# Kernel tuning notes

Hardware: AMD Instinct MI355X
Metric: run time of the kernel (lower is better)

Reference implementation:

```python
import jax, jax.numpy as jnp
import numpy as np

C = 64          # channels
L = 2           # GRU layers
DEC_STEPS = 35


def setup_inputs() -> dict:
    key = jax.random.key(0)
    ks = jax.random.split(key, 10)
    B, S = 2048, 512
    s = 0.1  # small init scale keeps gates in linear-ish region
    return {
        "pulse":    jax.random.normal(ks[0], (B, S, 2), dtype=jnp.float32),
        "dense1_w": jax.random.normal(ks[1], (C, 2), dtype=jnp.float32) * s,
        "dense1_b": jax.random.normal(ks[2], (C,), dtype=jnp.float32) * s,
        "dense2_w": jax.random.normal(ks[3], (2, C), dtype=jnp.float32) * s,
        "dense2_b": jax.random.normal(ks[4], (2,), dtype=jnp.float32) * s,
        "Wih":      jax.random.normal(ks[5], (L, 3 * C, C), dtype=jnp.float32) * s,
        "Whh":      jax.random.normal(ks[6], (L, 3 * C, C), dtype=jnp.float32) * s,
        "bih":      jax.random.normal(ks[7], (L, 3 * C), dtype=jnp.float32) * s,
        "bhh":      jax.random.normal(ks[8], (L, 3 * C), dtype=jnp.float32) * s,
        "embed":    jax.random.normal(ks[9], (1, C), dtype=jnp.float32) * s,
    }


def _gru_cell(x, h, wih, whh, bi, bh):
    # PyTorch GRU cell math (gate order r, z, n)
    gi = x @ wih.T + bi   # [B, 3C]
    gh = h @ whh.T + bh   # [B, 3C]
    ir, iz, inn = jnp.split(gi, 3, axis=-1)
    hr, hz, hn = jnp.split(gh, 3, axis=-1)
    r = jax.nn.sigmoid(ir + hr)
    z = jax.nn.sigmoid(iz + hz)
    n = jnp.tanh(inn + r * hn)
    return (1.0 - z) * n + z * h


def _multi_step(h_stack, x, Wih, Whh, bih, bhh):
    # One timestep through L stacked GRU layers. h_stack: [L, B, C]
    new_h = []
    inp = x
    for l in range(L):
        hl = _gru_cell(inp, h_stack[l], Wih[l], Whh[l], bih[l], bhh[l])
        new_h.append(hl)
        inp = hl
    return jnp.stack(new_h), inp  # (new state stack, top-layer output)


def reference(pulse, dense1_w, dense1_b, dense2_w, dense2_b, Wih, Whh, bih, bhh, embed):
    B = pulse.shape[0]
    # dense1 then time-major [S, B, C]
    x = pulse @ dense1_w.T + dense1_b
    x = jnp.transpose(x, (1, 0, 2))
    h0 = jnp.zeros((L, B, C), dtype=x.dtype)

    def enc_step(h, xt):
        h2, _ = _multi_step(h, xt, Wih, Whh, bih, bhh)
        return h2, None

    hT, _ = jax.lax.scan(enc_step, h0, x)  # encoder final state [L, B, C]

    sos = jnp.broadcast_to(embed[0], (B, C))  # embedding of token 0

    def dec_step(carry, _):
        latest, h = carry
        h2, out = _multi_step(h, latest, Wih, Whh, bih, bhh)
        return (out, h2), out

    _, outs = jax.lax.scan(dec_step, (sos, hT), None, length=DEC_STEPS)  # [35, B, C]

    # dense2 on decoder outputs; slicing pred[:, 1:, :] in the source drops the
    # sos position, which equals applying dense2 to the 35 decoder outputs only.
    pred = jnp.transpose(outs, (1, 0, 2)) @ dense2_w.T + dense2_b  # [B, 35, 2]
    return pred
```

## Files before the change

kernel.cpp:

```cpp
#include <hip/hip_runtime.h>
#include <math.h>


#define CCH  64
#define GG   192
#define SEQ  512
#define DECS 35
#define BT   8
#define NTH  512
#define NW   8
#define RSTR 20
#define STG_SH  (16 * 17 * 8)

typedef __attribute__((ext_vector_type(8))) short bf16x8;
typedef __attribute__((ext_vector_type(4))) float f32x4;

__device__ __forceinline__ short f2b(float f) {
  union { float f; unsigned u; } v; v.f = f;
  unsigned r = v.u + 0x7fffu + ((v.u >> 16) & 1u);
  return (short)(r >> 16);
}
__device__ __forceinline__ float sigf(float x) { return 1.0f / (1.0f + __expf(-x)); }
__device__ __forceinline__ float tanhfast(float x) {
  float t = __expf(-2.0f * fabsf(x));
  float r = (1.0f - t) / (1.0f + t);
  return copysignf(r, x);
}
__device__ __forceinline__ int stoff(int row, int k) {
  return ((k >> 3) * 17 + row) * 8 + (k & 7);
}

extern "C" __global__ void __launch_bounds__(NTH, 2)
gru_fused2(const float* __restrict__ pulse,
           const float* __restrict__ d1w,
           const float* __restrict__ d1b,
           const float* __restrict__ d2w,
           const float* __restrict__ d2b,
           const float* __restrict__ Wih,
           const float* __restrict__ Whh,
           const float* __restrict__ bih,
           const float* __restrict__ bhh,
           const float* __restrict__ embed,
           float* __restrict__ out)
{
  __shared__ __align__(16) unsigned short stA[STG_SH];
  __shared__ __align__(16) unsigned short stC[STG_SH];
  __shared__ __align__(16) float scr[NW * 32 * RSTR];
  __shared__ float red[NW * 16];

  const int tid = threadIdx.x;
  const int wid = tid >> 6;
  const int l   = tid & 63;
  const int lm  = l & 15;
  const int lg  = l >> 4;
  const int ob  = l >> 3;
  const int ocl = l & 7;
  const int och = wid * 8 + ocl;
  const int bgb = blockIdx.x * BT;

  for (int i = tid; i < STG_SH; i += NTH) { stA[i] = 0; stC[i] = 0; }

  const float* Wih0 = Wih;
  const float* Whh0 = Whh;
  const float* Wih1 = Wih + GG * CCH;
  const float* Whh1 = Whh + GG * CCH;
  bf16x8 bA[2][4], bC[2][4];
#pragma unroll
  for (int t = 0; t < 2; ++t) {
    const int cc = t * 16 + lm;
    const int g  = cc >> 3;
    const int ch = wid * 8 + (cc & 7);
#pragma unroll
    for (int s = 0; s < 4; ++s) {
#pragma unroll
      for (int e = 0; e < 8; ++e) {
        int kk = 32 * s + 8 * lg + e;
        float va = 0.f, vc = 0.f;
        if (g < 3) {
          int row = g * CCH + ch;
          va = (kk < 64) ? Wih0[row * CCH + kk] : Whh0[row * CCH + kk - 64];
          vc = (kk < 64) ? Wih1[row * CCH + kk] : Whh1[row * CCH + kk - 64];
        }
        bA[t][s][e] = f2b(va);
        bC[t][s][e] = f2b(vc);
      }
    }
  }

  float A0[3], A1[3], C0[3], bi0_[3], bh0_[3], bi1_[3], bh1_[3];
#pragma unroll
  for (int g = 0; g < 3; ++g) {
    int row = g * CCH + och;
    float a0 = 0.f, a1 = 0.f, cc = 0.f;
    for (int k = 0; k < CCH; ++k) {
      float wv = Wih0[row * CCH + k];
      a0 += wv * d1w[2 * k];
      a1 += wv * d1w[2 * k + 1];
      cc += wv * d1b[k];
    }
    A0[g] = a0; A1[g] = a1; C0[g] = cc + bih[row];
    bi0_[g] = bih[row];      bh0_[g] = bhh[row];
    bi1_[g] = bih[GG + row]; bh1_[g] = bhh[GG + row];
  }
  const float w20 = d2w[och], w21 = d2w[CCH + och];
  const float o_b0 = d2b[0], o_b1 = d2b[1];
  float h0 = 0.f, h1 = 0.f;
  short hb0 = 0, hb1 = 0;

  float* ws = scr + wid * 32 * RSTR;
  __syncthreads();

  for (int t = 0; t < SEQ; ++t) {
    stC[stoff(8 + ob, 64 + och)] = hb1;
    float2 pv = *(const float2*)(pulse + ((size_t)(bgb + ob) * SEQ + t) * 2);
    {
      f32x4 a0 = {0.f, 0.f, 0.f, 0.f}, a1 = {0.f, 0.f, 0.f, 0.f};
#pragma unroll
      for (int s = 2; s < 4; ++s) {
        bf16x8 af = *(const bf16x8*)&stA[((s * 4 + lg) * 17 + lm) * 8];
        a0 = __builtin_amdgcn_mfma_f32_16x16x32_bf16(af, bA[0][s], a0, 0, 0, 0);
        a1 = __builtin_amdgcn_mfma_f32_16x16x32_bf16(af, bA[1][s], a1, 0, 0, 0);
      }
      *(f32x4*)(ws + (0 * 16 + lm) * RSTR + lg * 4) = a0;
      *(f32x4*)(ws + (1 * 16 + lm) * RSTR + lg * 4) = a1;
    }
    {
      float ghR = ws[(0 * 8 + ocl) * RSTR + 8 + ob];
      float ghZ = ws[(1 * 8 + ocl) * RSTR + 8 + ob];
      float ghN = ws[(2 * 8 + ocl) * RSTR + 8 + ob];
      float giR = pv.x * A0[0] + pv.y * A1[0] + C0[0];
      float giZ = pv.x * A0[1] + pv.y * A1[1] + C0[1];
      float giN = pv.x * A0[2] + pv.y * A1[2] + C0[2];
      float r = sigf(giR + ghR + bh0_[0]);
      float z = sigf(giZ + ghZ + bh0_[1]);
      float nn = tanhfast(giN + r * (ghN + bh0_[2]));
      h0 = (1.f - z) * nn + z * h0;
      hb0 = f2b(h0);
      stC[stoff(ob, och)] = hb0;
    }
    __syncthreads();

    stA[stoff(8 + ob, 64 + och)] = hb0;
    {
      f32x4 a0 = {0.f, 0.f, 0.f, 0.f}, a1 = {0.f, 0.f, 0.f, 0.f};
#pragma unroll
      for (int s = 0; s < 4; ++s) {
        bf16x8 af = *(const bf16x8*)&stC[((s * 4 + lg) * 17 + lm) * 8];
        a0 = __builtin_amdgcn_mfma_f32_16x16x32_bf16(af, bC[0][s], a0, 0, 0, 0);
        a1 = __builtin_amdgcn_mfma_f32_16x16x32_bf16(af, bC[1][s], a1, 0, 0, 0);
      }
      *(f32x4*)(ws + (0 * 16 + lm) * RSTR + lg * 4) = a0;
      *(f32x4*)(ws + (1 * 16 + lm) * RSTR + lg * 4) = a1;
    }
    {
      float aR = ws[(0 * 8 + ocl) * RSTR + ob];
      float aZ = ws[(1 * 8 + ocl) * RSTR + ob];
      float aN = ws[(2 * 8 + ocl) * RSTR + ob];
      float hR = ws[(0 * 8 + ocl) * RSTR + 8 + ob];
      float hZ = ws[(1 * 8 + ocl) * RSTR + 8 + ob];
      float hN = ws[(2 * 8 + ocl) * RSTR + 8 + ob];
      float r = sigf(aR + hR + bi1_[0] + bh1_[0]);
      float z = sigf(aZ + hZ + bi1_[1] + bh1_[1]);
      float nn = tanhfast(aN + bi1_[2] + r * (hN + bh1_[2]));
      h1 = (1.f - z) * nn + z * h1;
      hb1 = f2b(h1);
    }
    __syncthreads();
  }

  stA[stoff(ob, och)] = f2b(embed[och]);
  __syncthreads();

  for (int d = 0; d < DECS; ++d) {
    stC[stoff(8 + ob, 64 + och)] = hb1;
    if (wid == 0 && l < 16 && d > 0) {
      int b = l >> 1, o = l & 1;
      float s = 0.f;
#pragma unroll
      for (int w = 0; w < NW; ++w) s += red[w * 16 + b * 2 + o];
      out[((size_t)(bgb + b) * DECS + (d - 1)) * 2 + o] = s + (o ? o_b1 : o_b0);
    }
    {
      f32x4 a0 = {0.f, 0.f, 0.f, 0.f}, a1 = {0.f, 0.f, 0.f, 0.f};
#pragma unroll
      for (int s = 0; s < 4; ++s) {
        bf16x8 af = *(const bf16x8*)&stA[((s * 4 + lg) * 17 + lm) * 8];
        a0 = __builtin_amdgcn_mfma_f32_16x16x32_bf16(af, bA[0][s], a0, 0, 0, 0);
        a1 = __builtin_amdgcn_mfma_f32_16x16x32_bf16(af, bA[1][s], a1, 0, 0, 0);
      }
      *(f32x4*)(ws + (0 * 16 + lm) * RSTR + lg * 4) = a0;
      *(f32x4*)(ws + (1 * 16 + lm) * RSTR + lg * 4) = a1;
    }
    {
      float aR = ws[(0 * 8 + ocl) * RSTR + ob];
      float aZ = ws[(1 * 8 + ocl) * RSTR + ob];
      float aN = ws[(2 * 8 + ocl) * RSTR + ob];
      float hR = ws[(0 * 8 + ocl) * RSTR + 8 + ob];
      float hZ = ws[(1 * 8 + ocl) * RSTR + 8 + ob];
      float hN = ws[(2 * 8 + ocl) * RSTR + 8 + ob];
      float r = sigf(aR + hR + bi0_[0] + bh0_[0]);
      float z = sigf(aZ + hZ + bi0_[1] + bh0_[1]);
      float nn = tanhfast(aN + bi0_[2] + r * (hN + bh0_[2]));
      h0 = (1.f - z) * nn + z * h0;
      hb0 = f2b(h0);
      stC[stoff(ob, och)] = hb0;
    }
    __syncthreads();

    stA[stoff(8 + ob, 64 + och)] = hb0;
    {
      f32x4 a0 = {0.f, 0.f, 0.f, 0.f}, a1 = {0.f, 0.f, 0.f, 0.f};
#pragma unroll
      for (int s = 0; s < 4; ++s) {
        bf16x8 af = *(const bf16x8*)&stC[((s * 4 + lg) * 17 + lm) * 8];
        a0 = __builtin_amdgcn_mfma_f32_16x16x32_bf16(af, bC[0][s], a0, 0, 0, 0);
        a1 = __builtin_amdgcn_mfma_f32_16x16x32_bf16(af, bC[1][s], a1, 0, 0, 0);
      }
      *(f32x4*)(ws + (0 * 16 + lm) * RSTR + lg * 4) = a0;
      *(f32x4*)(ws + (1 * 16 + lm) * RSTR + lg * 4) = a1;
    }
    {
      float aR = ws[(0 * 8 + ocl) * RSTR + ob];
      float aZ = ws[(1 * 8 + ocl) * RSTR + ob];
      float aN = ws[(2 * 8 + ocl) * RSTR + ob];
      float hR = ws[(0 * 8 + ocl) * RSTR + 8 + ob];
      float hZ = ws[(1 * 8 + ocl) * RSTR + 8 + ob];
      float hN = ws[(2 * 8 + ocl) * RSTR + 8 + ob];
      float r = sigf(aR + hR + bi1_[0] + bh1_[0]);
      float z = sigf(aZ + hZ + bi1_[1] + bh1_[1]);
      float nn = tanhfast(aN + bi1_[2] + r * (hN + bh1_[2]));
      h1 = (1.f - z) * nn + z * h1;
      hb1 = f2b(h1);
      stA[stoff(ob, och)] = hb1;
      float p0 = h1 * w20, p1 = h1 * w21;
      p0 += __shfl_xor(p0, 1); p0 += __shfl_xor(p0, 2); p0 += __shfl_xor(p0, 4);
      p1 += __shfl_xor(p1, 1); p1 += __shfl_xor(p1, 2); p1 += __shfl_xor(p1, 4);
      if (ocl == 0) {
        red[wid * 16 + ob * 2 + 0] = p0;
        red[wid * 16 + ob * 2 + 1] = p1;
      }
    }
    __syncthreads();
  }

  if (wid == 0 && l < 16) {
    int b = l >> 1, o = l & 1;
    float s = 0.f;
#pragma unroll
    for (int w = 0; w < NW; ++w) s += red[w * 16 + b * 2 + o];
    out[((size_t)(bgb + b) * DECS + (DECS - 1)) * 2 + o] = s + (o ? o_b1 : o_b0);
  }
}

extern "C" void kernel_launch(void* const* d_in, const int* in_sizes, int n_in,
                              void* d_out, int out_size, void* d_ws, size_t ws_size,
                              hipStream_t stream) {
  const float* pulse = (const float*)d_in[0];
  const float* d1w   = (const float*)d_in[1];
  const float* d1b   = (const float*)d_in[2];
  const float* d2w   = (const float*)d_in[3];
  const float* d2b   = (const float*)d_in[4];
  const float* Wih   = (const float*)d_in[5];
  const float* Whh   = (const float*)d_in[6];
  const float* bih   = (const float*)d_in[7];
  const float* bhh   = (const float*)d_in[8];
  const float* emb   = (const float*)d_in[9];
  float* out = (float*)d_out;

  int B = in_sizes[0] / (SEQ * 2);
  gru_fused2<<<B / BT, NTH, 0, stream>>>(pulse, d1w, d1b, d2w, d2b,
                                         Wih, Whh, bih, bhh, emb, out);
}
```

Baseline: 607.8 us.

## Swap MFMA operands so gate outputs land in lanes, dropping LDS scratch

The MFMA operands are swapped (weights as A, hidden state as B), and the weight rows are permuted so each lane's accumulator holds the r, z and n gate pre-activations for one channel and batch element. This removes the per-step round trip through the LDS scratch buffer (store the accumulators, then gather them back) in both GRU layers. In exchange the hidden state is written twice into the staging buffer, because the 8 batch rows are duplicated across 16 columns, which halves useful MFMA throughput. Biases are also pre-summed. Numerics change slightly because the layer-1 input and hidden r/z terms are now summed inside the MFMA.

```diff
diff --git a/kernel.cpp b/kernel.cpp
--- a/kernel.cpp
+++ b/kernel.cpp
@@ -9,8 +9,7 @@
 #define BT   8
 #define NTH  512
 #define NW   8
-#define RSTR 20
-#define STG_SH  (16 * 17 * 8)
+#define STG_SH (16 * 17 * 8)
 
 typedef __attribute__((ext_vector_type(8))) short bf16x8;
 typedef __attribute__((ext_vector_type(4))) float f32x4;
@@ -26,26 +25,25 @@
   float r = (1.0f - t) / (1.0f + t);
   return copysignf(r, x);
 }
-__device__ __forceinline__ int stoff(int row, int k) {
-  return ((k >> 3) * 17 + row) * 8 + (k & 7);
+__device__ __forceinline__ int stoff(int col, int k) {
+  return ((k >> 3) * 17 + col) * 8 + (k & 7);
 }
 
 extern "C" __global__ void __launch_bounds__(NTH, 2)
-gru_fused2(const float* __restrict__ pulse,
-           const float* __restrict__ d1w,
-           const float* __restrict__ d1b,
-           const float* __restrict__ d2w,
-           const float* __restrict__ d2b,
-           const float* __restrict__ Wih,
-           const float* __restrict__ Whh,
-           const float* __restrict__ bih,
-           const float* __restrict__ bhh,
-           const float* __restrict__ embed,
-           float* __restrict__ out)
+gru_lane(const float* __restrict__ pulse,
+         const float* __restrict__ d1w,
+         const float* __restrict__ d1b,
+         const float* __restrict__ d2w,
+         const float* __restrict__ d2b,
+         const float* __restrict__ Wih,
+         const float* __restrict__ Whh,
+         const float* __restrict__ bih,
+         const float* __restrict__ bhh,
+         const float* __restrict__ embed,
+         float* __restrict__ out)
 {
   __shared__ __align__(16) unsigned short stA[STG_SH];
   __shared__ __align__(16) unsigned short stC[STG_SH];
-  __shared__ __align__(16) float scr[NW * 32 * RSTR];
   __shared__ float red[NW * 16];
 
   const int tid = threadIdx.x;
@@ -53,9 +51,8 @@
   const int l   = tid & 63;
   const int lm  = l & 15;
   const int lg  = l >> 4;
-  const int ob  = l >> 3;
-  const int ocl = l & 7;
-  const int och = wid * 8 + ocl;
+  const int b   = lm & 7;
+  const int ch  = wid * 8 + ((lm >> 3) << 2) + lg;
   const int bgb = blockIdx.x * BT;
 
   for (int i = tid; i < STG_SH; i += NTH) { stA[i] = 0; stC[i] = 0; }
@@ -64,22 +61,27 @@
   const float* Whh0 = Whh;
   const float* Wih1 = Wih + GG * CCH;
   const float* Whh1 = Whh + GG * CCH;
+  const int sub = lm & 3;
   bf16x8 bA[2][4], bC[2][4];
 #pragma unroll
   for (int t = 0; t < 2; ++t) {
-    const int cc = t * 16 + lm;
-    const int g  = cc >> 3;
-    const int ch = wid * 8 + (cc & 7);
+    const int wch = wid * 8 + t * 4 + (lm >> 2);
+    const int rr  = (sub == 0 ? wch : (sub == 1 ? 64 + wch : 128 + wch));
 #pragma unroll
     for (int s = 0; s < 4; ++s) {
 #pragma unroll
       for (int e = 0; e < 8; ++e) {
         int kk = 32 * s + 8 * lg + e;
-        float va = 0.f, vc = 0.f;
-        if (g < 3) {
-          int row = g * CCH + ch;
-          va = (kk < 64) ? Wih0[row * CCH + kk] : Whh0[row * CCH + kk - 64];
-          vc = (kk < 64) ? Wih1[row * CCH + kk] : Whh1[row * CCH + kk - 64];
+        float va, vc;
+        if (sub == 2) {
+          va = kk < 64 ? Wih0[rr * CCH + kk] : 0.f;
+          vc = kk < 64 ? Wih1[rr * CCH + kk] : 0.f;
+        } else if (sub == 3) {
+          va = kk < 64 ? 0.f : Whh0[rr * CCH + kk - 64];
+          vc = kk < 64 ? 0.f : Whh1[rr * CCH + kk - 64];
+        } else {
+          va = kk < 64 ? Wih0[rr * CCH + kk] : Whh0[rr * CCH + kk - 64];
+          vc = kk < 64 ? Wih1[rr * CCH + kk] : Whh1[rr * CCH + kk - 64];
         }
         bA[t][s][e] = f2b(va);
         bC[t][s][e] = f2b(vc);
@@ -87,10 +89,10 @@
     }
   }
 
-  float A0[3], A1[3], C0[3], bi0_[3], bh0_[3], bi1_[3], bh1_[3];
+  float A0f[3], A1f[3], C0f[3];
 #pragma unroll
   for (int g = 0; g < 3; ++g) {
-    int row = g * CCH + och;
+    int row = g * CCH + ch;
     float a0 = 0.f, a1 = 0.f, cc = 0.f;
     for (int k = 0; k < CCH; ++k) {
       float wv = Wih0[row * CCH + k];
@@ -98,157 +100,140 @@
       a1 += wv * d1w[2 * k + 1];
       cc += wv * d1b[k];
     }
-    A0[g] = a0; A1[g] = a1; C0[g] = cc + bih[row];
-    bi0_[g] = bih[row];      bh0_[g] = bhh[row];
-    bi1_[g] = bih[GG + row]; bh1_[g] = bhh[GG + row];
-  }
-  const float w20 = d2w[och], w21 = d2w[CCH + och];
-  const float o_b0 = d2b[0], o_b1 = d2b[1];
+    A0f[g] = a0; A1f[g] = a1; C0f[g] = cc + bih[row];
+  }
+  const float bh0r = bhh[ch], bh0z = bhh[64 + ch], bh0n = bhh[128 + ch];
+  const float b0r = bih[ch] + bh0r, b0z = bih[64 + ch] + bh0z;
+  const float bi0n = bih[128 + ch];
+  const float b1r = bih[GG + ch] + bhh[GG + ch];
+  const float b1z = bih[GG + 64 + ch] + bhh[GG + 64 + ch];
+  const float bi1n = bih[GG + 128 + ch], bh1n = bhh[GG + 128 + ch];
+  const float w2a = d2w[ch], w2b = d2w[CCH + ch];
+  const float d2b0 = d2b[0], d2b1 = d2b[1];
   float h0 = 0.f, h1 = 0.f;
   short hb0 = 0, hb1 = 0;
 
-  float* ws = scr + wid * 32 * RSTR;
+  const float* prow = pulse + (size_t)(bgb + b) * SEQ * 2;
   __syncthreads();
 
   for (int t = 0; t < SEQ; ++t) {
-    stC[stoff(8 + ob, 64 + och)] = hb1;
-    float2 pv = *(const float2*)(pulse + ((size_t)(bgb + ob) * SEQ + t) * 2);
-    {
-      f32x4 a0 = {0.f, 0.f, 0.f, 0.f}, a1 = {0.f, 0.f, 0.f, 0.f};
-#pragma unroll
-      for (int s = 2; s < 4; ++s) {
-        bf16x8 af = *(const bf16x8*)&stA[((s * 4 + lg) * 17 + lm) * 8];
-        a0 = __builtin_amdgcn_mfma_f32_16x16x32_bf16(af, bA[0][s], a0, 0, 0, 0);
-        a1 = __builtin_amdgcn_mfma_f32_16x16x32_bf16(af, bA[1][s], a1, 0, 0, 0);
-      }
-      *(f32x4*)(ws + (0 * 16 + lm) * RSTR + lg * 4) = a0;
-      *(f32x4*)(ws + (1 * 16 + lm) * RSTR + lg * 4) = a1;
-    }
-    {
-      float ghR = ws[(0 * 8 + ocl) * RSTR + 8 + ob];
-      float ghZ = ws[(1 * 8 + ocl) * RSTR + 8 + ob];
-      float ghN = ws[(2 * 8 + ocl) * RSTR + 8 + ob];
-      float giR = pv.x * A0[0] + pv.y * A1[0] + C0[0];
-      float giZ = pv.x * A0[1] + pv.y * A1[1] + C0[1];
-      float giN = pv.x * A0[2] + pv.y * A1[2] + C0[2];
-      float r = sigf(giR + ghR + bh0_[0]);
-      float z = sigf(giZ + ghZ + bh0_[1]);
-      float nn = tanhfast(giN + r * (ghN + bh0_[2]));
+    stC[stoff(b, 64 + ch)] = hb1;
+    stC[stoff(8 + b, 64 + ch)] = hb1;
+    float2 pv = *(const float2*)(prow + 2 * t);
+    f32x4 a0 = {0.f, 0.f, 0.f, 0.f}, a1 = {0.f, 0.f, 0.f, 0.f};
+#pragma unroll
+    for (int s = 2; s < 4; ++s) {
+      bf16x8 af = *(const bf16x8*)&stA[((s * 4 + lg) * 17 + lm) * 8];
+      a0 = __builtin_amdgcn_mfma_f32_16x16x32_bf16(bA[0][s], af, a0, 0, 0, 0);
+      a1 = __builtin_amdgcn_mfma_f32_16x16x32_bf16(bA[1][s], af, a1, 0, 0, 0);
+    }
+    {
+      f32x4 g = (lm < 8) ? a0 : a1;
+      float fr = pv.x * A0f[0] + pv.y * A1f[0] + C0f[0];
+      float fz = pv.x * A0f[1] + pv.y * A1f[1] + C0f[1];
+      float fn = pv.x * A0f[2] + pv.y * A1f[2] + C0f[2];
+      float r = sigf(fr + g[0] + bh0r);
+      float z = sigf(fz + g[1] + bh0z);
+      float nn = tanhfast(fn + r * (g[3] + bh0n));
       h0 = (1.f - z) * nn + z * h0;
       hb0 = f2b(h0);
-      stC[stoff(ob, och)] = hb0;
-    }
-    __syncthreads();
-
-    stA[stoff(8 + ob, 64 + och)] = hb0;
-    {
-      f32x4 a0 = {0.f, 0.f, 0.f, 0.f}, a1 = {0.f, 0.f, 0.f, 0.f};
-#pragma unroll
-      for (int s = 0; s < 4; ++s) {
-        bf16x8 af = *(const bf16x8*)&stC[((s * 4 + lg) * 17 + lm) * 8];
-        a0 = __builtin_amdgcn_mfma_f32_16x16x32_bf16(af, bC[0][s], a0, 0, 0, 0);
-        a1 = __builtin_amdgcn_mfma_f32_16x16x32_bf16(af, bC[1][s], a1, 0, 0, 0);
-      }
-      *(f32x4*)(ws + (0 * 16 + lm) * RSTR + lg * 4) = a0;
-      *(f32x4*)(ws + (1 * 16 + lm) * RSTR + lg * 4) = a1;
-    }
-    {
-      float aR = ws[(0 * 8 + ocl) * RSTR + ob];
-      float aZ = ws[(1 * 8 + ocl) * RSTR + ob];
-      float aN = ws[(2 * 8 + ocl) * RSTR + ob];
-      float hR = ws[(0 * 8 + ocl) * RSTR + 8 + ob];
-      float hZ = ws[(1 * 8 + ocl) * RSTR + 8 + ob];
-      float hN = ws[(2 * 8 + ocl) * RSTR + 8 + ob];
-      float r = sigf(aR + hR + bi1_[0] + bh1_[0]);
-      float z = sigf(aZ + hZ + bi1_[1] + bh1_[1]);
-      float nn = tanhfast(aN + bi1_[2] + r * (hN + bh1_[2]));
+      stC[stoff(b, ch)] = hb0;
+      stC[stoff(8 + b, ch)] = hb0;
+    }
+    __syncthreads();
+
+    stA[stoff(b, 64 + ch)] = hb0;
+    stA[stoff(8 + b, 64 + ch)] = hb0;
+    f32x4 c0 = {0.f, 0.f, 0.f, 0.f}, c1 = {0.f, 0.f, 0.f, 0.f};
+#pragma unroll
+    for (int s = 0; s < 4; ++s) {
+      bf16x8 cf = *(const bf16x8*)&stC[((s * 4 + lg) * 17 + lm) * 8];
+      c0 = __builtin_amdgcn_mfma_f32_16x16x32_bf16(bC[0][s], cf, c0, 0, 0, 0);
+      c1 = __builtin_amdgcn_mfma_f32_16x16x32_bf16(bC[1][s], cf, c1, 0, 0, 0);
+    }
+    {
+      f32x4 g = (lm < 8) ? c0 : c1;
+      float r = sigf(g[0] + b1r);
+      float z = sigf(g[1] + b1z);
+      float nn = tanhfast(g[2] + bi1n + r * (g[3] + bh1n));
       h1 = (1.f - z) * nn + z * h1;
       hb1 = f2b(h1);
     }
     __syncthreads();
   }
 
-  stA[stoff(ob, och)] = f2b(embed[och]);
+  {
+    short eb = f2b(embed[ch]);
+    stA[stoff(b, ch)] = eb;
+    stA[stoff(8 + b, ch)] = eb;
+  }
   __syncthreads();
 
   for (int d = 0; d < DECS; ++d) {
-    stC[stoff(8 + ob, 64 + och)] = hb1;
+    stC[stoff(b, 64 + ch)] = hb1;
+    stC[stoff(8 + b, 64 + ch)] = hb1;
     if (wid == 0 && l < 16 && d > 0) {
-      int b = l >> 1, o = l & 1;
+      int bb = l >> 1, o = l & 1;
       float s = 0.f;
 #pragma unroll
-      for (int w = 0; w < NW; ++w) s += red[w * 16 + b * 2 + o];
-      out[((size_t)(bgb + b) * DECS + (d - 1)) * 2 + o] = s + (o ? o_b1 : o_b0);
-    }
-    {
-      f32x4 a0 = {0.f, 0.f, 0.f, 0.f}, a1 = {0.f, 0.f, 0.f, 0.f};
-#pragma unroll
-      for (int s = 0; s < 4; ++s) {
-        bf16x8 af = *(const bf16x8*)&stA[((s * 4 + lg) * 17 + lm) * 8];
-        a0 = __builtin_amdgcn_mfma_f32_16x16x32_bf16(af, bA[0][s], a0, 0, 0, 0);
-        a1 = __builtin_amdgcn_mfma_f32_16x16x32_bf16(af, bA[1][s], a1, 0, 0, 0);
-      }
-      *(f32x4*)(ws + (0 * 16 + lm) * RSTR + lg * 4) = a0;
-      *(f32x4*)(ws + (1 * 16 + lm) * RSTR + lg * 4) = a1;
-    }
-    {
-      float aR = ws[(0 * 8 + ocl) * RSTR + ob];
-      float aZ = ws[(1 * 8 + ocl) * RSTR + ob];
-      float aN = ws[(2 * 8 + ocl) * RSTR + ob];
-      float hR = ws[(0 * 8 + ocl) * RSTR + 8 + ob];
-      float hZ = ws[(1 * 8 + ocl) * RSTR + 8 + ob];
-      float hN = ws[(2 * 8 + ocl) * RSTR + 8 + ob];
-      float r = sigf(aR + hR + bi0_[0] + bh0_[0]);
-      float z = sigf(aZ + hZ + bi0_[1] + bh0_[1]);
-      float nn = tanhfast(aN + bi0_[2] + r * (hN + bh0_[2]));
+      for (int w = 0; w < NW; ++w) s += red[w * 16 + bb * 2 + o];
+      out[((size_t)(bgb + bb) * DECS + (d - 1)) * 2 + o] = s + (o ? d2b1 : d2b0);
+    }
+    f32x4 a0 = {0.f, 0.f, 0.f, 0.f}, a1 = {0.f, 0.f, 0.f, 0.f};
+#pragma unroll
+    for (int s = 0; s < 4; ++s) {
+      bf16x8 af = *(const bf16x8*)&stA[((s * 4 + lg) * 17 + lm) * 8];
+      a0 = __builtin_amdgcn_mfma_f32_16x16x32_bf16(bA[0][s], af, a0, 0, 0, 0);
+      a1 = __builtin_amdgcn_mfma_f32_16x16x32_bf16(bA[1][s], af, a1, 0, 0, 0);
+    }
+    {
+      f32x4 g = (lm < 8) ? a0 : a1;
+      float r = sigf(g[0] + b0r);
+      float z = sigf(g[1] + b0z);
+      float nn = tanhfast(g[2] + bi0n + r * (g[3] + bh0n));
       h0 = (1.f - z) * nn + z * h0;
       hb0 = f2b(h0);
-      stC[stoff(ob, och)] = hb0;
-    }
-    __syncthreads();
-
-    stA[stoff(8 + ob, 64 + och)] = hb0;
-    {
-      f32x4 a0 = {0.f, 0.f, 0.f, 0.f}, a1 = {0.f, 0.f, 0.f, 0.f};
-#pragma unroll
-      for (int s = 0; s < 4; ++s) {
-        bf16x8 af = *(const bf16x8*)&stC[((s * 4 + lg) * 17 + lm) * 8];
-        a0 = __builtin_amdgcn_mfma_f32_16x16x32_bf16(af, bC[0][s], a0, 0, 0, 0);
-        a1 = __builtin_amdgcn_mfma_f32_16x16x32_bf16(af, bC[1][s], a1, 0, 0, 0);
-      }
-      *(f32x4*)(ws + (0 * 16 + lm) * RSTR + lg * 4) = a0;
-      *(f32x4*)(ws + (1 * 16 + lm) * RSTR + lg * 4) = a1;
-    }
-    {
-      float aR = ws[(0 * 8 + ocl) * RSTR + ob];
-      float aZ = ws[(1 * 8 + ocl) * RSTR + ob];
-      float aN = ws[(2 * 8 + ocl) * RSTR + ob];
-      float hR = ws[(0 * 8 + ocl) * RSTR + 8 + ob];
-      float hZ = ws[(1 * 8 + ocl) * RSTR + 8 + ob];
-      float hN = ws[(2 * 8 + ocl) * RSTR + 8 + ob];
-      float r = sigf(aR + hR + bi1_[0] + bh1_[0]);
-      float z = sigf(aZ + hZ + bi1_[1] + bh1_[1]);
-      float nn = tanhfast(aN + bi1_[2] + r * (hN + bh1_[2]));
+      stC[stoff(b, ch)] = hb0;
+      stC[stoff(8 + b, ch)] = hb0;
+    }
+    __syncthreads();
+
+    stA[stoff(b, 64 + ch)] = hb0;
+    stA[stoff(8 + b, 64 + ch)] = hb0;
+    f32x4 c0 = {0.f, 0.f, 0.f, 0.f}, c1 = {0.f, 0.f, 0.f, 0.f};
+#pragma unroll
+    for (int s = 0; s < 4; ++s) {
+      bf16x8 cf = *(const bf16x8*)&stC[((s * 4 + lg) * 17 + lm) * 8];
+      c0 = __builtin_amdgcn_mfma_f32_16x16x32_bf16(bC[0][s], cf, c0, 0, 0, 0);
+      c1 = __builtin_amdgcn_mfma_f32_16x16x32_bf16(bC[1][s], cf, c1, 0, 0, 0);
+    }
+    {
+      f32x4 g = (lm < 8) ? c0 : c1;
+      float r = sigf(g[0] + b1r);
+      float z = sigf(g[1] + b1z);
+      float nn = tanhfast(g[2] + bi1n + r * (g[3] + bh1n));
       h1 = (1.f - z) * nn + z * h1;
       hb1 = f2b(h1);
-      stA[stoff(ob, och)] = hb1;
-      float p0 = h1 * w20, p1 = h1 * w21;
-      p0 += __shfl_xor(p0, 1); p0 += __shfl_xor(p0, 2); p0 += __shfl_xor(p0, 4);
-      p1 += __shfl_xor(p1, 1); p1 += __shfl_xor(p1, 2); p1 += __shfl_xor(p1, 4);
-      if (ocl == 0) {
-        red[wid * 16 + ob * 2 + 0] = p0;
-        red[wid * 16 + ob * 2 + 1] = p1;
+      stA[stoff(b, ch)] = hb1;
+      stA[stoff(8 + b, ch)] = hb1;
+      float p0 = h1 * w2a, p1 = h1 * w2b;
+      p0 += __shfl_xor(p0, 8);  p1 += __shfl_xor(p1, 8);
+      p0 += __shfl_xor(p0, 16); p1 += __shfl_xor(p1, 16);
+      p0 += __shfl_xor(p0, 32); p1 += __shfl_xor(p1, 32);
+      if (l < 8) {
+        red[wid * 16 + b * 2 + 0] = p0;
+        red[wid * 16 + b * 2 + 1] = p1;
       }
     }
     __syncthreads();
   }
 
   if (wid == 0 && l < 16) {
-    int b = l >> 1, o = l & 1;
+    int bb = l >> 1, o = l & 1;
     float s = 0.f;
 #pragma unroll
-    for (int w = 0; w < NW; ++w) s += red[w * 16 + b * 2 + o];
-    out[((size_t)(bgb + b) * DECS + (DECS - 1)) * 2 + o] = s + (o ? o_b1 : o_b0);
+    for (int w = 0; w < NW; ++w) s += red[w * 16 + bb * 2 + o];
+    out[((size_t)(bgb + bb) * DECS + (DECS - 1)) * 2 + o] = s + (o ? d2b1 : d2b0);
   }
 }
 
@@ -268,6 +253,6 @@
   float* out = (float*)d_out;
 
   int B = in_sizes[0] / (SEQ * 2);
-  gru_fused2<<<B / BT, NTH, 0, stream>>>(pulse, d1w, d1b, d2w, d2b,
-                                         Wih, Whh, bih, bhh, emb, out);
-}
+  gru_lane<<<B / BT, NTH, 0, stream>>>(pulse, d1w, d1b, d2w, d2b,
+                                       Wih, Whh, bih, bhh, emb, out);
+}
```

Result: faster. 577.0 us (-5.1%).
